# Performance work log

Measured on AMD Instinct MI355X. Metric: run time of the kernel, lower is better.

Reference implementation:

```python
import jax, jax.numpy as jnp
import numpy as np

V, E, HL, HH, T_STEPS, N_STEPS = 32000, 768, 1024, 768, 5, 3
B, S = 8, 256
EPS = 1e-5


def _ln(x, g, b):
    m = jnp.mean(x, axis=-1, keepdims=True)
    v = jnp.var(x, axis=-1, keepdims=True)
    return (x - m) * jax.lax.rsqrt(v + EPS) * g + b


def _gru(x, h, Wi, bi, Wh, bh, lni_g, lni_b, lnh_g, lnh_b):
    # Wi: [3, in_dim, H]; gates stacked in order (r, z, n)
    xi = jnp.einsum('bd,kdh->kbh', x, Wi) + bi[:, None, :]
    hi = jnp.einsum('bh,khg->kbg', h, Wh) + bh[:, None, :]
    xi = _ln(xi, lni_g[:, None, :], lni_b[:, None, :])
    hi = _ln(hi, lnh_g[:, None, :], lnh_b[:, None, :])
    r = jax.nn.sigmoid(xi[0] + hi[0])
    z = jax.nn.sigmoid(xi[1] + hi[1])
    n = jnp.tanh(xi[2] + r * hi[2])
    return (1.0 - z) * n + z * h


def setup_inputs() -> dict:
    key = jax.random.key(0)
    ks = jax.random.split(key, 12)
    lin = E + HH  # low-level cell input dim (x concat h_h)

    def xavier(k, shape, fan_in, fan_out):
        lim = float(np.sqrt(6.0 / (fan_in + fan_out)))
        return jax.random.uniform(k, shape, jnp.float32, -lim, lim)

    inp = {
        'input_ids': jax.random.randint(ks[0], (B, S), 0, V),
        'emb': xavier(ks[1], (V, E), V, E),
        'ln_emb_g': jnp.ones((E,), jnp.float32),
        'ln_emb_b': jnp.zeros((E,), jnp.float32),
        'low_Wi': xavier(ks[2], (3, lin, HL), lin, HL),
        'low_bi': jnp.zeros((3, HL), jnp.float32),
        'low_Wh': xavier(ks[3], (3, HL, HL), HL, HL),
        'low_bh': jnp.zeros((3, HL), jnp.float32),
        'low_lni_g': jnp.ones((3, HL), jnp.float32),
        'low_lni_b': jnp.zeros((3, HL), jnp.float32),
        'low_lnh_g': jnp.ones((3, HL), jnp.float32),
        'low_lnh_b': jnp.zeros((3, HL), jnp.float32),
        'high_Wi': xavier(ks[4], (3, HL, HH), HL, HH),
        'high_bi': jnp.zeros((3, HH), jnp.float32),
        'high_Wh': xavier(ks[5], (3, HH, HH), HH, HH),
        'high_bh': jnp.zeros((3, HH), jnp.float32),
        'high_lni_g': jnp.ones((3, HH), jnp.float32),
        'high_lni_b': jnp.zeros((3, HH), jnp.float32),
        'high_lnh_g': jnp.ones((3, HH), jnp.float32),
        'high_lnh_b': jnp.zeros((3, HH), jnp.float32),
        'Wout': xavier(ks[6], (HH, V), HH, V),
        'bout': jnp.zeros((V,), jnp.float32),
    }
    return inp


def reference(input_ids, emb, ln_emb_g, ln_emb_b,
              low_Wi, low_bi, low_Wh, low_bh,
              low_lni_g, low_lni_b, low_lnh_g, low_lnh_b,
              high_Wi, high_bi, high_Wh, high_bh,
              high_lni_g, high_lni_b, high_lnh_g, high_lnh_b,
              Wout, bout):
    b = input_ids.shape[0]
    h_l0 = jnp.zeros((b, HL), jnp.float32)
    h_h0 = jnp.zeros((b, HH), jnp.float32)

    def step(carry, ids_t):
        h_l, h_h = carry
        x = _ln(emb[ids_t], ln_emb_g, ln_emb_b)  # [B, E]
        for _ in range(N_STEPS):
            for _ in range(T_STEPS):
                h_l = _gru(jnp.concatenate([x, h_h], axis=-1), h_l,
                           low_Wi, low_bi, low_Wh, low_bh,
                           low_lni_g, low_lni_b, low_lnh_g, low_lnh_b)
            h_h = _gru(h_l, h_h,
                       high_Wi, high_bi, high_Wh, high_bh,
                       high_lni_g, high_lni_b, high_lnh_g, high_lnh_b)
        logits_t = h_h @ Wout + bout  # [B, V]
        return (h_l, h_h), logits_t

    _, logits = jax.lax.scan(step, (h_l0, h_h0), input_ids.T)  # [S, B, V]
    return jnp.transpose(logits, (1, 0, 2))  # [B, S, V]
```

## Files before the change

kernel.cpp:

```cpp
#include <hip/hip_runtime.h>
#include <hip/hip_bf16.h>


#define NWG 128
#define NTH 256
#define EPSV 1e-5f

typedef __attribute__((ext_vector_type(4))) float f32x4;
typedef __attribute__((ext_vector_type(8))) short short8;
typedef unsigned long long u64;

struct PArgs {
  const int* ids; const float* emb; const float* lng; const float* lnb;
  const float* lWi; const float* lbi; const float* lWh; const float* lbh;
  const float* llig; const float* llib; const float* llhg; const float* llhb;
  const float* hWi; const float* hbi; const float* hWh; const float* hbh;
  const float* hlig; const float* hlib; const float* hlhg; const float* hlhb;
  int* arr; int* rel; u64* statsG; u64* sredG; float* hlR; float* hhR;
  __hip_bfloat16* hist; float* WiT; float* hWiT; float* hWhT;
};

__device__ __forceinline__ float sigm(float x) { return 1.f / (1.f + __expf(-x)); }
__device__ __forceinline__ float tanh_f(float x) {
  x = fminf(15.f, fmaxf(-15.f, x));
  float e = __expf(2.f * x);
  return (e - 1.f) / (e + 1.f);
}
__device__ __forceinline__ void ast(float* p, float v) {
  __hip_atomic_store(p, v, __ATOMIC_RELAXED, __HIP_MEMORY_SCOPE_AGENT);
}
__device__ __forceinline__ int aldi(const int* p) {
  return __hip_atomic_load(p, __ATOMIC_RELAXED, __HIP_MEMORY_SCOPE_AGENT);
}
__device__ __forceinline__ u64 aldu(const u64* p) {
  return __hip_atomic_load(p, __ATOMIC_RELAXED, __HIP_MEMORY_SCOPE_AGENT);
}
__device__ __forceinline__ void astu(u64* p, u64 v) {
  __hip_atomic_store(p, v, __ATOMIC_RELAXED, __HIP_MEMORY_SCOPE_AGENT);
}
__device__ __forceinline__ void asti(int* p, int v) {
  __hip_atomic_store(p, v, __ATOMIC_RELAXED, __HIP_MEMORY_SCOPE_AGENT);
}
__device__ __forceinline__ void ald4x2(const float* p0, const float* p1,
                                       float4& a, float4& b) {
  asm volatile(
      "global_load_dwordx4 %0, %2, off sc1\n\t"
      "global_load_dwordx4 %1, %3, off sc1\n\t"
      "s_waitcnt vmcnt(0)"
      : "=&v"(a), "=&v"(b)
      : "v"(p0), "v"(p1)
      : "memory");
}
__device__ __forceinline__ void ald4x4(const float* p0, const float* p1,
                                       const float* p2, const float* p3,
                                       float4& a, float4& b, float4& c, float4& d) {
  asm volatile(
      "global_load_dwordx4 %0, %4, off sc1\n\t"
      "global_load_dwordx4 %1, %5, off sc1\n\t"
      "global_load_dwordx4 %2, %6, off sc1\n\t"
      "global_load_dwordx4 %3, %7, off sc1\n\t"
      "s_waitcnt vmcnt(0)"
      : "=&v"(a), "=&v"(b), "=&v"(c), "=&v"(d)
      : "v"(p0), "v"(p1), "v"(p2), "v"(p3)
      : "memory");
}
__device__ __forceinline__ void ald4x8(const float* p0, const float* p1,
                                       const float* p2, const float* p3,
                                       const float* p4, const float* p5,
                                       const float* p6, const float* p7,
                                       float4& a, float4& b, float4& c, float4& d,
                                       float4& e, float4& f, float4& g, float4& h) {
  asm volatile(
      "global_load_dwordx4 %0, %8, off sc1\n\t"
      "global_load_dwordx4 %1, %9, off sc1\n\t"
      "global_load_dwordx4 %2, %10, off sc1\n\t"
      "global_load_dwordx4 %3, %11, off sc1\n\t"
      "global_load_dwordx4 %4, %12, off sc1\n\t"
      "global_load_dwordx4 %5, %13, off sc1\n\t"
      "global_load_dwordx4 %6, %14, off sc1\n\t"
      "global_load_dwordx4 %7, %15, off sc1\n\t"
      "s_waitcnt vmcnt(0)"
      : "=&v"(a), "=&v"(b), "=&v"(c), "=&v"(d),
        "=&v"(e), "=&v"(f), "=&v"(g), "=&v"(h)
      : "v"(p0), "v"(p1), "v"(p2), "v"(p3),
        "v"(p4), "v"(p5), "v"(p6), "v"(p7)
      : "memory");
}

__global__ void __launch_bounds__(NTH) hrm_recur(PArgs P) {
  const int tid = threadIdx.x;

  if (blockIdx.x == NWG) {
    __shared__ float mbuf[192][4];
    __shared__ int mok;
    auto mevent = [&](int e, int lo, int n, float invD, int par) -> bool {
      if (tid < 64) {
        const u64* ap = (const u64*)P.arr + tid;
        int lim = 1 << 22, good = 1;
        for (;;) {
          u64 v = aldu(ap);
          int a0 = (int)(unsigned)(v & 0xffffffffull);
          int a1 = (int)(unsigned)(v >> 32);
          if (__all(a0 >= e && a1 >= e)) break;
          if (--lim == 0) { good = 0; break; }
          __builtin_amdgcn_s_sleep(1);
        }
        if (tid == 0) mok = good;
      }
      __syncthreads();
      bool good = (mok != 0);
      if (good && n > 0) {
        const int rpn = n >> 1;
        const int Q = (n == 48) ? 8 : 16;
        const int wpq = 128 / Q;
        if (tid < rpn * Q) {
          int rp = (lo >> 1) + tid / Q, q = tid % Q;
          const float* b0 = (const float*)(P.statsG + (size_t)par * 128 * 48);
          float4 s; s.x = 0.f; s.y = 0.f; s.z = 0.f; s.w = 0.f;
          #pragma unroll
          for (int blk = 0; blk < 2; ++blk) {
            if (blk == 1 && wpq == 8) break;
            int w0 = q * wpq + blk * 8;
            float4 t0,t1,t2,t3,t4,t5,t6,t7;
            ald4x8(b0 + ((size_t)(w0+0)*48 + rp*2)*2, b0 + ((size_t)(w0+1)*48 + rp*2)*2,
                   b0 + ((size_t)(w0+2)*48 + rp*2)*2, b0 + ((size_t)(w0+3)*48 + rp*2)*2,
                   b0 + ((size_t)(w0+4)*48 + rp*2)*2, b0 + ((size_t)(w0+5)*48 + rp*2)*2,
                   b0 + ((size_t)(w0+6)*48 + rp*2)*2, b0 + ((size_t)(w0+7)*48 + rp*2)*2,
                   t0,t1,t2,t3,t4,t5,t6,t7);
            s.x += t0.x+t1.x+t2.x+t3.x+t4.x+t5.x+t6.x+t7.x;
            s.y += t0.y+t1.y+t2.y+t3.y+t4.y+t5.y+t6.y+t7.y;
            s.z += t0.z+t1.z+t2.z+t3.z+t4.z+t5.z+t6.z+t7.z;
            s.w += t0.w+t1.w+t2.w+t3.w+t4.w+t5.w+t6.w+t7.w;
          }
          mbuf[tid][0] = s.x; mbuf[tid][1] = s.y; mbuf[tid][2] = s.z; mbuf[tid][3] = s.w;
        }
        __syncthreads();
        if (tid < n) {
          int rpl = tid >> 1, comp = tid & 1;
          const int Q2 = (n == 48) ? 8 : 16;
          float s1 = 0.f, s2 = 0.f;
          for (int q = 0; q < Q2; ++q) {
            s1 += mbuf[rpl * Q2 + q][comp * 2 + 0];
            s2 += mbuf[rpl * Q2 + q][comp * 2 + 1];
          }
          float m = s1 * invD;
          float rs = rsqrtf(s2 * invD - m * m + EPSV);
          union { u64 u; float f[2]; } c; c.f[0] = m; c.f[1] = rs;
          astu(P.sredG + (size_t)par * 48 + lo + tid, c.u);
        }
        asm volatile("s_waitcnt vmcnt(0)" ::: "memory");
        __syncthreads();
      }
      int pub = good ? e : (1 << 30);
      if (tid < 8) asti(P.rel + tid * 16, pub);
      return good;
    };

    if (!mevent(1, 0, 0, 0.f, 0)) return;
    int rr = 0;
    #pragma unroll 1
    for (int t = 0; t < 256; ++t) {
      #pragma unroll 1
      for (int nn = 0; nn < 3; ++nn) {
        ++rr;
        if (!mevent(2*rr, 0, 48, 1.f/1024.f, rr & 1)) return;
        if (!mevent(2*rr + 1, 0, 0, 0.f, 0)) return;
        #pragma unroll 1
        for (int it = 1; it < 5; ++it) {
          ++rr;
          if (!mevent(2*rr, 24, 24, 1.f/1024.f, rr & 1)) return;
          if (!mevent(2*rr + 1, 0, 0, 0.f, 0)) return;
        }
        ++rr;
        if (!mevent(2*rr, 0, 48, 1.f/768.f, rr & 1)) return;
        if (!mevent(2*rr + 1, 0, 0, 0.f, 0)) return;
      }
    }
    return;
  }

  __shared__ float WhS[24 * 1024];
  __shared__ float Bb[8 * 1024];
  __shared__ float XW[24 * 8];
  __shared__ float xiNs[24 * 8];
  __shared__ float stg[2][24 * 8];
  __shared__ float sred[96];
  __shared__ float xm[8], xrs[8];
  __shared__ int idsh[8];
  __shared__ int okf;

  const int wg = blockIdx.x;
  const int ks = tid & 31, cg = tid >> 5;
  const int lj8 = wg * 8, lj6 = wg * 6;
  const int rep = wg & 3;

  auto arrive = [&](int e) {
    asm volatile("s_waitcnt vmcnt(0)" ::: "memory");
    __syncthreads();
    if (tid == 0) asti(P.arr + wg, e);
  };
  auto wwait = [&](int e) -> bool {
    if (tid == 0) {
      const int* rp = P.rel + (wg & 7) * 16;
      int lim = 1 << 22, v = 0;
      do {
        v = aldi(rp);
        if (v >= e) break;
        __builtin_amdgcn_s_sleep(1);
      } while (--lim);
      okf = (lim != 0 && v < (1 << 29)) ? 1 : 0;
    }
    __syncthreads();
    return okf != 0;
  };

  auto stage_hl = [&]() {
    const float* base = P.hlR + (size_t)rep * 8192 + tid * 4;
    float4 t0,t1,t2,t3,t4,t5,t6,t7;
    ald4x8(base + 0*1024, base + 1*1024, base + 2*1024, base + 3*1024,
           base + 4*1024, base + 5*1024, base + 6*1024, base + 7*1024,
           t0,t1,t2,t3,t4,t5,t6,t7);
    *(float4*)&Bb[0*1024 + tid*4] = t0; *(float4*)&Bb[1*1024 + tid*4] = t1;
    *(float4*)&Bb[2*1024 + tid*4] = t2; *(float4*)&Bb[3*1024 + tid*4] = t3;
    *(float4*)&Bb[4*1024 + tid*4] = t4; *(float4*)&Bb[5*1024 + tid*4] = t5;
    *(float4*)&Bb[6*1024 + tid*4] = t6; *(float4*)&Bb[7*1024 + tid*4] = t7;
  };
  auto stage_hh = [&]() {
    const float* base = P.hhR + (size_t)rep * 6144;
    int bi[6], ki[6];
    #pragma unroll
    for (int i = 0; i < 6; ++i) {
      int c = i * 256 + tid; int b = c / 192; int k = (c - b * 192) * 4;
      bi[i] = b; ki[i] = k;
    }
    float4 t0,t1,t2,t3,t4,t5;
    ald4x4(base + bi[0]*768 + ki[0], base + bi[1]*768 + ki[1],
           base + bi[2]*768 + ki[2], base + bi[3]*768 + ki[3], t0,t1,t2,t3);
    ald4x2(base + bi[4]*768 + ki[4], base + bi[5]*768 + ki[5], t4,t5);
    *(float4*)&Bb[bi[0]*1024 + ki[0]] = t0; *(float4*)&Bb[bi[1]*1024 + ki[1]] = t1;
    *(float4*)&Bb[bi[2]*1024 + ki[2]] = t2; *(float4*)&Bb[bi[3]*1024 + ki[3]] = t3;
    *(float4*)&Bb[bi[4]*1024 + ki[4]] = t4; *(float4*)&Bb[bi[5]*1024 + ki[5]] = t5;
  };

  auto gemm_lowh = [&](float (&acc)[3][8]) {
    const int c0 = cg * 3;
    const float* w0p = &WhS[(c0 + 0) * 1024];
    const float* w1p = &WhS[(c0 + 1) * 1024];
    const float* w2p = &WhS[(c0 + 2) * 1024];
    #pragma unroll
    for (int i = 0; i < 8; ++i) {
      int k = i * 128 + ks * 4;
      float4 w0 = *(const float4*)&w0p[k];
      float4 w1 = *(const float4*)&w1p[k];
      float4 w2 = *(const float4*)&w2p[k];
      #pragma unroll
      for (int b = 0; b < 8; ++b) {
        float4 h = *(const float4*)&Bb[b * 1024 + k];
        acc[0][b] += w0.x*h.x + w0.y*h.y + w0.z*h.z + w0.w*h.w;
        acc[1][b] += w1.x*h.x + w1.y*h.y + w1.z*h.z + w1.w*h.w;
        acc[2][b] += w2.x*h.x + w2.y*h.y + w2.z*h.z + w2.w*h.w;
      }
    }
  };
  auto gemm_xih = [&](float (&acc)[3][8]) {
    const float* wp[3];
    #pragma unroll
    for (int cc = 0; cc < 3; ++cc) {
      int c = cg * 3 + cc; int g = c >> 3, jj = c & 7;
      wp[cc] = P.WiT + ((size_t)g * 1024 + lj8 + jj) * 1536 + 768;
    }
    #pragma unroll
    for (int i = 0; i < 6; ++i) {
      int k = i * 128 + ks * 4;
      float4 w0 = *(const float4*)&wp[0][k];
      float4 w1 = *(const float4*)&wp[1][k];
      float4 w2 = *(const float4*)&wp[2][k];
      #pragma unroll
      for (int b = 0; b < 8; ++b) {
        float4 h = *(const float4*)&Bb[b * 1024 + k];
        acc[0][b] += w0.x*h.x + w0.y*h.y + w0.z*h.z + w0.w*h.w;
        acc[1][b] += w1.x*h.x + w1.y*h.y + w1.z*h.z + w1.w*h.w;
        acc[2][b] += w2.x*h.x + w2.y*h.y + w2.z*h.z + w2.w*h.w;
      }
    }
  };
  auto gemm_hxi = [&](float (&acc)[3][8]) {
    if (cg >= 6) return;
    const float* wp[3];
    #pragma unroll
    for (int cc = 0; cc < 3; ++cc) {
      int c = cg * 3 + cc; int g = c / 6, jj = c % 6;
      wp[cc] = P.hWiT + ((size_t)g * 768 + lj6 + jj) * 1024;
    }
    #pragma unroll
    for (int i = 0; i < 8; ++i) {
      int k = i * 128 + ks * 4;
      float4 w0 = *(const float4*)&wp[0][k];
      float4 w1 = *(const float4*)&wp[1][k];
      float4 w2 = *(const float4*)&wp[2][k];
      #pragma unroll
      for (int b = 0; b < 8; ++b) {
        float4 h = *(const float4*)&Bb[b * 1024 + k];
        acc[0][b] += w0.x*h.x + w0.y*h.y + w0.z*h.z + w0.w*h.w;
        acc[1][b] += w1.x*h.x + w1.y*h.y + w1.z*h.z + w1.w*h.w;
        acc[2][b] += w2.x*h.x + w2.y*h.y + w2.z*h.z + w2.w*h.w;
      }
    }
  };
  auto gemm_hhh = [&](float (&acc)[3][8]) {
    if (cg >= 6) return;
    const float* wp[3];
    #pragma unroll
    for (int cc = 0; cc < 3; ++cc) {
      int c = cg * 3 + cc; int g = c / 6, jj = c % 6;
      wp[cc] = P.hWhT + ((size_t)g * 768 + lj6 + jj) * 768;
    }
    #pragma unroll
    for (int i = 0; i < 6; ++i) {
      int k = i * 128 + ks * 4;
      float4 w0 = *(const float4*)&wp[0][k];
      float4 w1 = *(const float4*)&wp[1][k];
      float4 w2 = *(const float4*)&wp[2][k];
      #pragma unroll
      for (int b = 0; b < 8; ++b) {
        float4 h = *(const float4*)&Bb[b * 1024 + k];
        acc[0][b] += w0.x*h.x + w0.y*h.y + w0.z*h.z + w0.w*h.w;
        acc[1][b] += w1.x*h.x + w1.y*h.y + w1.z*h.z + w1.w*h.w;
        acc[2][b] += w2.x*h.x + w2.y*h.y + w2.z*h.z + w2.w*h.w;
      }
    }
  };

  auto redstage = [&](float (&acc)[3][8], int set, const float* bias, int dim,
                      int perg, int jb, bool addXW) {
    #pragma unroll
    for (int cc = 0; cc < 3; ++cc)
      #pragma unroll
      for (int b = 0; b < 8; ++b) {
        float v = acc[cc][b];
        #pragma unroll
        for (int m = 1; m < 32; m <<= 1) v += __shfl_xor(v, m, 64);
        acc[cc][b] = v;
      }
    if ((tid & 31) == 0) {
      int cgl = tid >> 5;
      #pragma unroll
      for (int cc = 0; cc < 3; ++cc) {
        int c = cgl * 3 + cc;
        if (c < perg * 3) {
          int g = (perg == 8) ? (c >> 3) : (c / 6);
          int jj = (perg == 8) ? (c & 7) : (c % 6);
          float bs = bias[g * dim + jb + jj];
          #pragma unroll
          for (int b = 0; b < 8; ++b) {
            float v = acc[cc][b] + bs;
            if (addXW) v += XW[c * 8 + b];
            stg[set][c * 8 + b] = v;
          }
        }
      }
    }
  };

  auto stats_put = [&](int par, int set, int perg) {
    if (tid < 24) {
      int g = tid >> 3, b = tid & 7;
      float s1 = 0.f, s2 = 0.f;
      for (int jj = 0; jj < perg; ++jj) {
        float v = stg[set][(g * perg + jj) * 8 + b];
        s1 += v; s2 += v * v;
      }
      union { u64 u; float f[2]; } c; c.f[0] = s1; c.f[1] = s2;
      astu(P.statsG + ((size_t)par * 128 + wg) * 48 + set * 24 + tid, c.u);
    }
  };
  auto sred_read = [&](int par, int lo, int n) {
    if (tid < n) {
      int row = lo + tid;
      union { u64 u; float f[2]; } c;
      c.u = aldu(P.sredG + (size_t)par * 48 + row);
      int set = row / 24, p = row % 24, g = p >> 3, b = p & 7;
      sred[set * 48 + g * 16 + b * 2] = c.f[0];
      sred[set * 48 + g * 16 + b * 2 + 1] = c.f[1];
    }
    __syncthreads();
  };

  auto gate_low = [&](bool isA) {
    if (tid < 64) {
      int jj = tid & 7, b = tid >> 3; int j = lj8 + jj;
      float xin[3], hin[3];
      #pragma unroll
      for (int g = 0; g < 3; ++g) {
        int c = g * 8 + jj;
        if (isA) {
          float m = sred[g * 16 + b * 2], rs = sred[g * 16 + b * 2 + 1];
          float v = (stg[0][c * 8 + b] - m) * rs * P.llig[g * 1024 + j] + P.llib[g * 1024 + j];
          xiNs[c * 8 + b] = v; xin[g] = v;
        } else {
          xin[g] = xiNs[c * 8 + b];
        }
        float m2 = sred[48 + g * 16 + b * 2], rs2 = sred[48 + g * 16 + b * 2 + 1];
        hin[g] = (stg[1][c * 8 + b] - m2) * rs2 * P.llhg[g * 1024 + j] + P.llhb[g * 1024 + j];
      }
      float rg = sigm(xin[0] + hin[0]);
      float zg = sigm(xin[1] + hin[1]);
      float ng = tanh_f(xin[2] + rg * hin[2]);
      float hold = Bb[b * 1024 + j];
      float hv = (1.f - zg) * ng + zg * hold;
      #pragma unroll
      for (int rp = 0; rp < 4; ++rp) ast(&P.hlR[rp * 8192 + b * 1024 + j], hv);
    }
  };

  auto gate_high = [&](int t, int nn) {
    if (tid < 48) {
      int jj = tid % 6, b = tid / 6; int j = lj6 + jj;
      float xin[3], hin[3];
      #pragma unroll
      for (int g = 0; g < 3; ++g) {
        int c = g * 6 + jj;
        float m = sred[g * 16 + b * 2], rs = sred[g * 16 + b * 2 + 1];
        xin[g] = (stg[0][c * 8 + b] - m) * rs * P.hlig[g * 768 + j] + P.hlib[g * 768 + j];
        float m2 = sred[48 + g * 16 + b * 2], rs2 = sred[48 + g * 16 + b * 2 + 1];
        hin[g] = (stg[1][c * 8 + b] - m2) * rs2 * P.hlhg[g * 768 + j] + P.hlhb[g * 768 + j];
      }
      float rg = sigm(xin[0] + hin[0]);
      float zg = sigm(xin[1] + hin[1]);
      float ng = tanh_f(xin[2] + rg * hin[2]);
      float hold = Bb[b * 1024 + j];
      float hv = (1.f - zg) * ng + zg * hold;
      #pragma unroll
      for (int rp = 0; rp < 4; ++rp) ast(&P.hhR[rp * 6144 + b * 768 + j], hv);
      if (nn == 2) P.hist[((size_t)t * 8 + b) * 768 + j] = __float2bfloat16(hv);
    }
  };

  auto xfun = [&](int tt) {
    int b = tid >> 5, u = tid & 31;
    if (tid < 8) idsh[tid] = P.ids[tid * 256 + tt];
    int id = P.ids[b * 256 + tt];
    const float* e = P.emb + (size_t)id * 768;
    float s1 = 0.f, s2 = 0.f;
    #pragma unroll
    for (int q = 0; q < 24; q += 4) {
      float4 v = *(const float4*)&e[u * 24 + q];
      s1 += v.x + v.y + v.z + v.w;
      s2 += v.x*v.x + v.y*v.y + v.z*v.z + v.w*v.w;
    }
    #pragma unroll
    for (int m = 1; m < 32; m <<= 1) { s1 += __shfl_xor(s1, m, 64); s2 += __shfl_xor(s2, m, 64); }
    if (u == 0) { float mm = s1 / 768.f; xm[b] = mm; xrs[b] = rsqrtf(s2 / 768.f - mm * mm + EPSV); }
    __syncthreads();
    float acc[3][8] = {};
    const float* wp[3];
    #pragma unroll
    for (int cc = 0; cc < 3; ++cc) {
      int c = cg * 3 + cc; int g = c >> 3, jj = c & 7;
      wp[cc] = P.WiT + ((size_t)g * 1024 + lj8 + jj) * 1536;
    }
    int idv[8];
    #pragma unroll
    for (int bb = 0; bb < 8; ++bb) idv[bb] = idsh[bb];
    #pragma unroll
    for (int i = 0; i < 6; ++i) {
      int k = i * 128 + ks * 4;
      float4 w0 = *(const float4*)&wp[0][k];
      float4 w1 = *(const float4*)&wp[1][k];
      float4 w2 = *(const float4*)&wp[2][k];
      float4 gam = *(const float4*)&P.lng[k];
      float4 bet = *(const float4*)&P.lnb[k];
      #pragma unroll
      for (int bb = 0; bb < 8; ++bb) {
        float4 xv = *(const float4*)&P.emb[(size_t)idv[bb] * 768 + k];
        float4 xn;
        xn.x = (xv.x - xm[bb]) * xrs[bb] * gam.x + bet.x;
        xn.y = (xv.y - xm[bb]) * xrs[bb] * gam.y + bet.y;
        xn.z = (xv.z - xm[bb]) * xrs[bb] * gam.z + bet.z;
        xn.w = (xv.w - xm[bb]) * xrs[bb] * gam.w + bet.w;
        acc[0][bb] += w0.x*xn.x + w0.y*xn.y + w0.z*xn.z + w0.w*xn.w;
        acc[1][bb] += w1.x*xn.x + w1.y*xn.y + w1.z*xn.z + w1.w*xn.w;
        acc[2][bb] += w2.x*xn.x + w2.y*xn.y + w2.z*xn.z + w2.w*xn.w;
      }
    }
    #pragma unroll
    for (int cc = 0; cc < 3; ++cc)
      #pragma unroll
      for (int bb = 0; bb < 8; ++bb) {
        float v = acc[cc][bb];
        #pragma unroll
        for (int m = 1; m < 32; m <<= 1) v += __shfl_xor(v, m, 64);
        acc[cc][bb] = v;
      }
    if ((tid & 31) == 0) {
      int cgl = tid >> 5;
      #pragma unroll
      for (int cc = 0; cc < 3; ++cc)
        #pragma unroll
        for (int bb = 0; bb < 8; ++bb)
          XW[(cgl * 3 + cc) * 8 + bb] = acc[cc][bb];
    }
    __syncthreads();
  };

  #pragma unroll 1
  for (int g = 0; g < 3; ++g)
    for (int it = 0; it < 6; ++it) {
      int k = it * 256 + tid;
      const float* src = P.lWi + ((size_t)g * 1536 + k) * 1024 + lj8;
      float4 v0 = *(const float4*)src; float4 v1 = *(const float4*)(src + 4);
      float vv[8] = {v0.x, v0.y, v0.z, v0.w, v1.x, v1.y, v1.z, v1.w};
      for (int jj = 0; jj < 8; ++jj)
        P.WiT[((size_t)g * 1024 + lj8 + jj) * 1536 + k] = vv[jj];
    }
  #pragma unroll 1
  for (int g = 0; g < 3; ++g)
    for (int it = 0; it < 4; ++it) {
      int k = it * 256 + tid;
      const float* src = P.hWi + ((size_t)g * 1024 + k) * 768 + lj6;
      float2 a = *(const float2*)src, b2v = *(const float2*)(src + 2), c2v = *(const float2*)(src + 4);
      float vv[6] = {a.x, a.y, b2v.x, b2v.y, c2v.x, c2v.y};
      for (int jj = 0; jj < 6; ++jj)
        P.hWiT[((size_t)g * 768 + lj6 + jj) * 1024 + k] = vv[jj];
    }
  #pragma unroll 1
  for (int g = 0; g < 3; ++g)
    for (int it = 0; it < 3; ++it) {
      int k = it * 256 + tid;
      const float* src = P.hWh + ((size_t)g * 768 + k) * 768 + lj6;
      float2 a = *(const float2*)src, b2v = *(const float2*)(src + 2), c2v = *(const float2*)(src + 4);
      float vv[6] = {a.x, a.y, b2v.x, b2v.y, c2v.x, c2v.y};
      for (int jj = 0; jj < 6; ++jj)
        P.hWhT[((size_t)g * 768 + lj6 + jj) * 768 + k] = vv[jj];
    }
  #pragma unroll 1
  for (int g = 0; g < 3; ++g)
    for (int it = 0; it < 4; ++it) {
      int k = it * 256 + tid;
      const float* src = P.lWh + ((size_t)g * 1024 + k) * 1024 + lj8;
      float4 v0 = *(const float4*)src; float4 v1 = *(const float4*)(src + 4);
      float vv[8] = {v0.x, v0.y, v0.z, v0.w, v1.x, v1.y, v1.z, v1.w};
      for (int jj = 0; jj < 8; ++jj) WhS[(g * 8 + jj) * 1024 + k] = vv[jj];
    }
  __syncthreads();
  xfun(0);
  arrive(1);
  bool alive = wwait(1);

  int rr = 0;
  #pragma unroll 1
  for (int t = 0; alive && t < 256; ++t) {
    #pragma unroll 1
    for (int nn = 0; nn < 3 && alive; ++nn) {
      ++rr; int par = rr & 1;
      {
        stage_hh(); __syncthreads();
        float accX[3][8] = {};
        gemm_xih(accX);
        redstage(accX, 0, P.lbi, 1024, 8, lj8, true);
        __syncthreads();
        stage_hl(); __syncthreads();
        float accH[3][8] = {};
        gemm_lowh(accH);
        redstage(accH, 1, P.lbh, 1024, 8, lj8, false);
        __syncthreads();
        stats_put(par, 0, 8); stats_put(par, 1, 8);
        arrive(2 * rr);
        alive = wwait(2 * rr); if (!alive) break;
        sred_read(par, 0, 48);
        gate_low(true);
        arrive(2 * rr + 1);
        alive = wwait(2 * rr + 1); if (!alive) break;
      }
      #pragma unroll 1
      for (int it = 1; it < 5 && alive; ++it) {
        ++rr; par = rr & 1;
        stage_hl(); __syncthreads();
        float acc2[3][8] = {};
        gemm_lowh(acc2);
        redstage(acc2, 1, P.lbh, 1024, 8, lj8, false);
        __syncthreads();
        stats_put(par, 1, 8);
        arrive(2 * rr);
        alive = wwait(2 * rr); if (!alive) break;
        sred_read(par, 24, 24);
        gate_low(false);
        arrive(2 * rr + 1);
        alive = wwait(2 * rr + 1); if (!alive) break;
      }
      if (!alive) break;
      ++rr; par = rr & 1;
      {
        stage_hl(); __syncthreads();
        float aX[3][8] = {};
        gemm_hxi(aX);
        redstage(aX, 0, P.hbi, 768, 6, lj6, false);
        __syncthreads();
        stage_hh(); __syncthreads();
        float aH[3][8] = {};
        gemm_hhh(aH);
        redstage(aH, 1, P.hbh, 768, 6, lj6, false);
        __syncthreads();
        stats_put(par, 0, 6); stats_put(par, 1, 6);
        arrive(2 * rr);
        alive = wwait(2 * rr); if (!alive) break;
        sred_read(par, 0, 48);
        gate_high(t, nn);
        if (nn == 2 && t < 255) { __syncthreads(); xfun(t + 1); }
        arrive(2 * rr + 1);
        alive = wwait(2 * rr + 1); if (!alive) break;
      }
    }
  }
}

__global__ void __launch_bounds__(256) wout_t(const float* __restrict__ W,
                                              __hip_bfloat16* __restrict__ WT) {
  __shared__ float T[64][65];
  int n0 = blockIdx.x * 64, k0 = blockIdx.y * 64;
  int tid = threadIdx.x;
  int lane16 = tid & 15, grp = tid >> 4;
  #pragma unroll
  for (int i = 0; i < 4; ++i) {
    int kl = i * 16 + grp; int nl = lane16 * 4;
    float4 v = *(const float4*)&W[(size_t)(k0 + kl) * 32000 + n0 + nl];
    T[kl][nl] = v.x; T[kl][nl + 1] = v.y; T[kl][nl + 2] = v.z; T[kl][nl + 3] = v.w;
  }
  __syncthreads();
  #pragma unroll
  for (int i = 0; i < 4; ++i) {
    int nl = i * 16 + grp; int kl = lane16 * 4;
    union { ushort4 v; __hip_bfloat16 h[4]; } u;
    for (int q = 0; q < 4; ++q) u.h[q] = __float2bfloat16(T[kl + q][nl]);
    *(ushort4*)&WT[(size_t)(n0 + nl) * 768 + k0 + kl] = u.v;
  }
}

__global__ void __launch_bounds__(256) logits_gemm(const __hip_bfloat16* __restrict__ Ah,
                                                   const __hip_bfloat16* __restrict__ Bt,
                                                   const float* __restrict__ bias,
                                                   float* __restrict__ out) {
  __shared__ short As[128 * 64];
  __shared__ short Bs[128 * 64];
  int m0 = blockIdx.y * 128, n0 = blockIdx.x * 128;
  int tid = threadIdx.x, lane = tid & 63, w = tid >> 6;
  int wr = w >> 1, wc = w & 1;
  int r16 = lane & 15, khalf = (lane >> 4) * 8;
  f32x4 acc[4][4];
  #pragma unroll
  for (int i = 0; i < 4; ++i)
    #pragma unroll
    for (int j = 0; j < 4; ++j)
      #pragma unroll
      for (int q = 0; q < 4; ++q) acc[i][j][q] = 0.f;

  for (int kt = 0; kt < 12; ++kt) {
    int k0 = kt * 64;
    __syncthreads();
    #pragma unroll
    for (int it = 0; it < 4; ++it) {
      int f = it * 2048 + tid * 8; int row = f >> 6, col = f & 63;
      *(uint4*)&As[f] = *(const uint4*)&Ah[(size_t)(m0 + row) * 768 + k0 + col];
      *(uint4*)&Bs[f] = *(const uint4*)&Bt[(size_t)(n0 + row) * 768 + k0 + col];
    }
    __syncthreads();
    #pragma unroll
    for (int kk = 0; kk < 64; kk += 32) {
      short8 af[4], bfr[4];
      #pragma unroll
      for (int i = 0; i < 4; ++i)
        af[i] = *(short8*)&As[(wr * 64 + i * 16 + r16) * 64 + kk + khalf];
      #pragma unroll
      for (int j = 0; j < 4; ++j)
        bfr[j] = *(short8*)&Bs[(wc * 64 + j * 16 + r16) * 64 + kk + khalf];
      #pragma unroll
      for (int i = 0; i < 4; ++i)
        #pragma unroll
        for (int j = 0; j < 4; ++j)
          acc[i][j] = __builtin_amdgcn_mfma_f32_16x16x32_bf16(af[i], bfr[j], acc[i][j], 0, 0, 0);
    }
  }
  #pragma unroll
  for (int i = 0; i < 4; ++i)
    #pragma unroll
    for (int j = 0; j < 4; ++j)
      #pragma unroll
      for (int q = 0; q < 4; ++q) {
        int m = m0 + wr * 64 + i * 16 + ((lane >> 4) * 4 + q);
        int n = n0 + wc * 64 + j * 16 + (lane & 15);
        out[(size_t)(m & 7) * 8192000 + (size_t)(m >> 3) * 32000 + n] =
            acc[i][j][q] + bias[n];
      }
}

extern "C" void kernel_launch(void* const* d_in, const int* in_sizes, int n_in,
                              void* d_out, int out_size, void* d_ws, size_t ws_size,
                              hipStream_t stream) {
  (void)in_sizes; (void)n_in; (void)out_size; (void)ws_size;
  char* wsb = (char*)d_ws;
  size_t off = 0;
  auto take = [&](size_t bytes) -> void* {
    void* p = wsb + off;
    off += (bytes + 1023) & ~(size_t)1023;
    return p;
  };
  int* arr      = (int*)take((size_t)128 * 4);
  int* rel      = (int*)take((size_t)8 * 16 * 4);
  float* hlR    = (float*)take((size_t)4 * 8 * 1024 * 4);
  float* hhR    = (float*)take((size_t)4 * 8 * 768 * 4);
  size_t state_bytes = off;
  u64* statsG   = (u64*)take((size_t)2 * 128 * 48 * 8);
  u64* sredG    = (u64*)take((size_t)2 * 48 * 8);
  __hip_bfloat16* hist = (__hip_bfloat16*)take((size_t)2048 * 768 * 2);
  float* WiT    = (float*)take((size_t)3 * 1024 * 1536 * 4);
  float* hWiT   = (float*)take((size_t)3 * 768 * 1024 * 4);
  float* hWhT   = (float*)take((size_t)3 * 768 * 768 * 4);
  __hip_bfloat16* WoutT = (__hip_bfloat16*)take((size_t)32000 * 768 * 2);

  hipMemsetAsync(d_ws, 0, state_bytes, stream);

  wout_t<<<dim3(500, 12), 256, 0, stream>>>((const float*)d_in[20], WoutT);

  PArgs A;
  A.ids = (const int*)d_in[0];   A.emb = (const float*)d_in[1];
  A.lng = (const float*)d_in[2]; A.lnb = (const float*)d_in[3];
  A.lWi = (const float*)d_in[4]; A.lbi = (const float*)d_in[5];
  A.lWh = (const float*)d_in[6]; A.lbh = (const float*)d_in[7];
  A.llig = (const float*)d_in[8];  A.llib = (const float*)d_in[9];
  A.llhg = (const float*)d_in[10]; A.llhb = (const float*)d_in[11];
  A.hWi = (const float*)d_in[12];  A.hbi = (const float*)d_in[13];
  A.hWh = (const float*)d_in[14];  A.hbh = (const float*)d_in[15];
  A.hlig = (const float*)d_in[16]; A.hlib = (const float*)d_in[17];
  A.hlhg = (const float*)d_in[18]; A.hlhb = (const float*)d_in[19];
  A.arr = arr; A.rel = rel; A.statsG = statsG; A.sredG = sredG;
  A.hlR = hlR; A.hhR = hhR;
  A.hist = hist; A.WiT = WiT; A.hWiT = hWiT; A.hWhT = hWhT;

  hrm_recur<<<NWG + 1, NTH, 0, stream>>>(A);

  logits_gemm<<<dim3(250, 16), 256, 0, stream>>>(hist, WoutT,
                                                 (const float*)d_in[21],
                                                 (float*)d_out);
}
```

Measured before the change: 70.98 ms.

## Centralize layernorm and gate computation in master block to halve grid barriers

Worker blocks now push raw pre-norm gate outputs to global buffers and arrive once per GRU step. The dedicated master block gathers the full vectors, computes layernorm statistics with wave shuffles, applies the gates, and broadcasts the new hidden state. This removes the second grid-wide barrier per step and the partial-statistics exchange. In exchange, the single master block serializes the elementwise gate work and adds global traffic for the raw vectors.

```diff
diff --git a/kernel.cpp b/kernel.cpp
--- a/kernel.cpp
+++ b/kernel.cpp
@@ -5,6 +5,7 @@
 #define NWG 128
 #define NTH 256
 #define EPSV 1e-5f
+#define NROUND 4608
 
 typedef __attribute__((ext_vector_type(4))) float f32x4;
 typedef __attribute__((ext_vector_type(8))) short short8;
@@ -16,7 +17,7 @@
   const float* llig; const float* llib; const float* llhg; const float* llhb;
   const float* hWi; const float* hbi; const float* hWh; const float* hbh;
   const float* hlig; const float* hlib; const float* hlhg; const float* hlhb;
-  int* arr; int* rel; u64* statsG; u64* sredG; float* hlR; float* hhR;
+  int* arr; int* rel; float* rawL; float* rawH; float* hlR; float* hhR;
   __hip_bfloat16* hist; float* WiT; float* hWiT; float* hWhT;
 };
 
@@ -26,43 +27,23 @@
   float e = __expf(2.f * x);
   return (e - 1.f) / (e + 1.f);
 }
-__device__ __forceinline__ void ast(float* p, float v) {
-  __hip_atomic_store(p, v, __ATOMIC_RELAXED, __HIP_MEMORY_SCOPE_AGENT);
-}
 __device__ __forceinline__ int aldi(const int* p) {
   return __hip_atomic_load(p, __ATOMIC_RELAXED, __HIP_MEMORY_SCOPE_AGENT);
 }
 __device__ __forceinline__ u64 aldu(const u64* p) {
   return __hip_atomic_load(p, __ATOMIC_RELAXED, __HIP_MEMORY_SCOPE_AGENT);
 }
+__device__ __forceinline__ void asti(int* p, int v) {
+  __hip_atomic_store(p, v, __ATOMIC_RELAXED, __HIP_MEMORY_SCOPE_AGENT);
+}
+__device__ __forceinline__ u64 pk2(float a, float b) {
+  union { u64 u; float f[2]; } c; c.f[0] = a; c.f[1] = b; return c.u;
+}
 __device__ __forceinline__ void astu(u64* p, u64 v) {
   __hip_atomic_store(p, v, __ATOMIC_RELAXED, __HIP_MEMORY_SCOPE_AGENT);
 }
-__device__ __forceinline__ void asti(int* p, int v) {
-  __hip_atomic_store(p, v, __ATOMIC_RELAXED, __HIP_MEMORY_SCOPE_AGENT);
-}
-__device__ __forceinline__ void ald4x2(const float* p0, const float* p1,
-                                       float4& a, float4& b) {
-  asm volatile(
-      "global_load_dwordx4 %0, %2, off sc1\n\t"
-      "global_load_dwordx4 %1, %3, off sc1\n\t"
-      "s_waitcnt vmcnt(0)"
-      : "=&v"(a), "=&v"(b)
-      : "v"(p0), "v"(p1)
-      : "memory");
-}
-__device__ __forceinline__ void ald4x4(const float* p0, const float* p1,
-                                       const float* p2, const float* p3,
-                                       float4& a, float4& b, float4& c, float4& d) {
-  asm volatile(
-      "global_load_dwordx4 %0, %4, off sc1\n\t"
-      "global_load_dwordx4 %1, %5, off sc1\n\t"
-      "global_load_dwordx4 %2, %6, off sc1\n\t"
-      "global_load_dwordx4 %3, %7, off sc1\n\t"
-      "s_waitcnt vmcnt(0)"
-      : "=&v"(a), "=&v"(b), "=&v"(c), "=&v"(d)
-      : "v"(p0), "v"(p1), "v"(p2), "v"(p3)
-      : "memory");
+__device__ __forceinline__ void ast2f(float* p, float a, float b) {
+  astu((u64*)p, pk2(a, b));
 }
 __device__ __forceinline__ void ald4x8(const float* p0, const float* p1,
                                        const float* p2, const float* p3,
@@ -86,108 +67,307 @@
         "v"(p4), "v"(p5), "v"(p6), "v"(p7)
       : "memory");
 }
+__device__ __forceinline__ void ald4x6(const float* p0, const float* p1,
+                                       const float* p2, const float* p3,
+                                       const float* p4, const float* p5,
+                                       float4& a, float4& b, float4& c,
+                                       float4& d, float4& e, float4& f) {
+  asm volatile(
+      "global_load_dwordx4 %0, %6, off sc1\n\t"
+      "global_load_dwordx4 %1, %7, off sc1\n\t"
+      "global_load_dwordx4 %2, %8, off sc1\n\t"
+      "global_load_dwordx4 %3, %9, off sc1\n\t"
+      "global_load_dwordx4 %4, %10, off sc1\n\t"
+      "global_load_dwordx4 %5, %11, off sc1\n\t"
+      "s_waitcnt vmcnt(0)"
+      : "=&v"(a), "=&v"(b), "=&v"(c), "=&v"(d), "=&v"(e), "=&v"(f)
+      : "v"(p0), "v"(p1), "v"(p2), "v"(p3), "v"(p4), "v"(p5)
+      : "memory");
+}
+__device__ __forceinline__ void ald4x4(const float* p0, const float* p1,
+                                       const float* p2, const float* p3,
+                                       float4& a, float4& b, float4& c, float4& d) {
+  asm volatile(
+      "global_load_dwordx4 %0, %4, off sc1\n\t"
+      "global_load_dwordx4 %1, %5, off sc1\n\t"
+      "global_load_dwordx4 %2, %6, off sc1\n\t"
+      "global_load_dwordx4 %3, %7, off sc1\n\t"
+      "s_waitcnt vmcnt(0)"
+      : "=&v"(a), "=&v"(b), "=&v"(c), "=&v"(d)
+      : "v"(p0), "v"(p1), "v"(p2), "v"(p3)
+      : "memory");
+}
+__device__ __forceinline__ void ald4x2(const float* p0, const float* p1,
+                                       float4& a, float4& b) {
+  asm volatile(
+      "global_load_dwordx4 %0, %2, off sc1\n\t"
+      "global_load_dwordx4 %1, %3, off sc1\n\t"
+      "s_waitcnt vmcnt(0)"
+      : "=&v"(a), "=&v"(b)
+      : "v"(p0), "v"(p1)
+      : "memory");
+}
 
 __global__ void __launch_bounds__(NTH) hrm_recur(PArgs P) {
+  __shared__ float smem[38920];
   const int tid = threadIdx.x;
 
   if (blockIdx.x == NWG) {
-    __shared__ float mbuf[192][4];
-    __shared__ int mok;
-    auto mevent = [&](int e, int lo, int n, float invD, int par) -> bool {
+    float* xiN = smem;
+    float* hL  = smem + 24576;
+    float* hH  = smem + 32768;
+    int* mokp  = (int*)(smem + 38912);
+    const int b = tid >> 5, l = tid & 31;
+
+    for (int i = tid; i < 8192; i += NTH) hL[i] = 0.f;
+    for (int i = tid; i < 6144; i += NTH) hH[i] = 0.f;
+    __syncthreads();
+    if (tid < 8) asti(P.rel + tid * 16, 1);
+
+    auto load_low_g = [&](int set, int g, float4 (&rv)[4][2]) {
+      const float* base = P.rawL + (((size_t)(set * 3 + g) * 8 + b) * 1024) + l * 8;
+      ald4x8(base, base + 4, base + 256, base + 260,
+             base + 512, base + 516, base + 768, base + 772,
+             rv[0][0], rv[0][1], rv[1][0], rv[1][1],
+             rv[2][0], rv[2][1], rv[3][0], rv[3][1]);
+    };
+    auto load_high_g = [&](int set, int g, float4 (&rv)[3][2]) {
+      const float* base = P.rawH + (((size_t)(set * 3 + g) * 8 + b) * 768) + l * 8;
+      ald4x6(base, base + 4, base + 256, base + 260, base + 512, base + 516,
+             rv[0][0], rv[0][1], rv[1][0], rv[1][1], rv[2][0], rv[2][1]);
+    };
+
+    #pragma unroll 1
+    for (int r = 1; r <= NROUND; ++r) {
       if (tid < 64) {
         const u64* ap = (const u64*)P.arr + tid;
-        int lim = 1 << 22, good = 1;
+        int lim = 1 << 22, g1 = 1;
         for (;;) {
           u64 v = aldu(ap);
           int a0 = (int)(unsigned)(v & 0xffffffffull);
           int a1 = (int)(unsigned)(v >> 32);
-          if (__all(a0 >= e && a1 >= e)) break;
-          if (--lim == 0) { good = 0; break; }
+          if (__all(a0 >= r && a1 >= r)) break;
+          if (--lim == 0) { g1 = 0; break; }
           __builtin_amdgcn_s_sleep(1);
         }
-        if (tid == 0) mok = good;
+        if (tid == 0) *mokp = g1;
       }
       __syncthreads();
-      bool good = (mok != 0);
-      if (good && n > 0) {
-        const int rpn = n >> 1;
-        const int Q = (n == 48) ? 8 : 16;
-        const int wpq = 128 / Q;
-        if (tid < rpn * Q) {
-          int rp = (lo >> 1) + tid / Q, q = tid % Q;
-          const float* b0 = (const float*)(P.statsG + (size_t)par * 128 * 48);
-          float4 s; s.x = 0.f; s.y = 0.f; s.z = 0.f; s.w = 0.f;
-          #pragma unroll
-          for (int blk = 0; blk < 2; ++blk) {
-            if (blk == 1 && wpq == 8) break;
-            int w0 = q * wpq + blk * 8;
-            float4 t0,t1,t2,t3,t4,t5,t6,t7;
-            ald4x8(b0 + ((size_t)(w0+0)*48 + rp*2)*2, b0 + ((size_t)(w0+1)*48 + rp*2)*2,
-                   b0 + ((size_t)(w0+2)*48 + rp*2)*2, b0 + ((size_t)(w0+3)*48 + rp*2)*2,
-                   b0 + ((size_t)(w0+4)*48 + rp*2)*2, b0 + ((size_t)(w0+5)*48 + rp*2)*2,
-                   b0 + ((size_t)(w0+6)*48 + rp*2)*2, b0 + ((size_t)(w0+7)*48 + rp*2)*2,
-                   t0,t1,t2,t3,t4,t5,t6,t7);
-            s.x += t0.x+t1.x+t2.x+t3.x+t4.x+t5.x+t6.x+t7.x;
-            s.y += t0.y+t1.y+t2.y+t3.y+t4.y+t5.y+t6.y+t7.y;
-            s.z += t0.z+t1.z+t2.z+t3.z+t4.z+t5.z+t6.z+t7.z;
-            s.w += t0.w+t1.w+t2.w+t3.w+t4.w+t5.w+t6.w+t7.w;
-          }
-          mbuf[tid][0] = s.x; mbuf[tid][1] = s.y; mbuf[tid][2] = s.z; mbuf[tid][3] = s.w;
+      if (!*mokp) { if (tid < 8) asti(P.rel + tid * 16, 1 << 30); return; }
+
+      const int ph = (r - 1) % 6;
+      const int nn = ((r - 1) / 6) % 3;
+      const int t  = (r - 1) / 18;
+
+      if (ph != 5) {
+        float mm[3], rs[3];
+        if (ph == 0) {
+          float4 rv[3][4][2];
+          #pragma unroll
+          for (int g = 0; g < 3; ++g) load_low_g(0, g, rv[g]);
+          #pragma unroll
+          for (int g = 0; g < 3; ++g) {
+            float s1 = 0.f, s2 = 0.f;
+            #pragma unroll
+            for (int q = 0; q < 4; ++q)
+              #pragma unroll
+              for (int h2 = 0; h2 < 2; ++h2) {
+                float4 v = rv[g][q][h2];
+                s1 += v.x + v.y + v.z + v.w;
+                s2 += v.x*v.x + v.y*v.y + v.z*v.z + v.w*v.w;
+              }
+            #pragma unroll
+            for (int m = 1; m < 32; m <<= 1) { s1 += __shfl_xor(s1, m, 64); s2 += __shfl_xor(s2, m, 64); }
+            float mean = s1 * (1.f / 1024.f);
+            mm[g] = mean; rs[g] = rsqrtf(s2 * (1.f / 1024.f) - mean * mean + EPSV);
+          }
+          #pragma unroll
+          for (int g = 0; g < 3; ++g)
+            #pragma unroll
+            for (int q = 0; q < 4; ++q) {
+              int j0 = q * 256 + l * 8;
+              float4 G0 = *(const float4*)&P.llig[g * 1024 + j0];
+              float4 G1 = *(const float4*)&P.llig[g * 1024 + j0 + 4];
+              float4 B0 = *(const float4*)&P.llib[g * 1024 + j0];
+              float4 B1 = *(const float4*)&P.llib[g * 1024 + j0 + 4];
+              float4 r0 = rv[g][q][0], r1 = rv[g][q][1];
+              float4 x0, x1;
+              x0.x = (r0.x - mm[g]) * rs[g] * G0.x + B0.x;
+              x0.y = (r0.y - mm[g]) * rs[g] * G0.y + B0.y;
+              x0.z = (r0.z - mm[g]) * rs[g] * G0.z + B0.z;
+              x0.w = (r0.w - mm[g]) * rs[g] * G0.w + B0.w;
+              x1.x = (r1.x - mm[g]) * rs[g] * G1.x + B1.x;
+              x1.y = (r1.y - mm[g]) * rs[g] * G1.y + B1.y;
+              x1.z = (r1.z - mm[g]) * rs[g] * G1.z + B1.z;
+              x1.w = (r1.w - mm[g]) * rs[g] * G1.w + B1.w;
+              *(float4*)&xiN[((size_t)g * 8 + b) * 1024 + j0] = x0;
+              *(float4*)&xiN[((size_t)g * 8 + b) * 1024 + j0 + 4] = x1;
+            }
         }
-        __syncthreads();
-        if (tid < n) {
-          int rpl = tid >> 1, comp = tid & 1;
-          const int Q2 = (n == 48) ? 8 : 16;
+        float4 rv[3][4][2];
+        #pragma unroll
+        for (int g = 0; g < 3; ++g) load_low_g(1, g, rv[g]);
+        #pragma unroll
+        for (int g = 0; g < 3; ++g) {
           float s1 = 0.f, s2 = 0.f;
-          for (int q = 0; q < Q2; ++q) {
-            s1 += mbuf[rpl * Q2 + q][comp * 2 + 0];
-            s2 += mbuf[rpl * Q2 + q][comp * 2 + 1];
-          }
-          float m = s1 * invD;
-          float rs = rsqrtf(s2 * invD - m * m + EPSV);
-          union { u64 u; float f[2]; } c; c.f[0] = m; c.f[1] = rs;
-          astu(P.sredG + (size_t)par * 48 + lo + tid, c.u);
+          #pragma unroll
+          for (int q = 0; q < 4; ++q)
+            #pragma unroll
+            for (int h2 = 0; h2 < 2; ++h2) {
+              float4 v = rv[g][q][h2];
+              s1 += v.x + v.y + v.z + v.w;
+              s2 += v.x*v.x + v.y*v.y + v.z*v.z + v.w*v.w;
+            }
+          #pragma unroll
+          for (int m = 1; m < 32; m <<= 1) { s1 += __shfl_xor(s1, m, 64); s2 += __shfl_xor(s2, m, 64); }
+          float mean = s1 * (1.f / 1024.f);
+          mm[g] = mean; rs[g] = rsqrtf(s2 * (1.f / 1024.f) - mean * mean + EPSV);
         }
-        asm volatile("s_waitcnt vmcnt(0)" ::: "memory");
-        __syncthreads();
-      }
-      int pub = good ? e : (1 << 30);
-      if (tid < 8) asti(P.rel + tid * 16, pub);
-      return good;
-    };
-
-    if (!mevent(1, 0, 0, 0.f, 0)) return;
-    int rr = 0;
-    #pragma unroll 1
-    for (int t = 0; t < 256; ++t) {
-      #pragma unroll 1
-      for (int nn = 0; nn < 3; ++nn) {
-        ++rr;
-        if (!mevent(2*rr, 0, 48, 1.f/1024.f, rr & 1)) return;
-        if (!mevent(2*rr + 1, 0, 0, 0.f, 0)) return;
-        #pragma unroll 1
-        for (int it = 1; it < 5; ++it) {
-          ++rr;
-          if (!mevent(2*rr, 24, 24, 1.f/1024.f, rr & 1)) return;
-          if (!mevent(2*rr + 1, 0, 0, 0.f, 0)) return;
+        #pragma unroll
+        for (int q = 0; q < 4; ++q) {
+          int j0 = q * 256 + l * 8;
+          float hin[3][8];
+          #pragma unroll
+          for (int g = 0; g < 3; ++g) {
+            float4 G0 = *(const float4*)&P.llhg[g * 1024 + j0];
+            float4 G1 = *(const float4*)&P.llhg[g * 1024 + j0 + 4];
+            float4 B0 = *(const float4*)&P.llhb[g * 1024 + j0];
+            float4 B1 = *(const float4*)&P.llhb[g * 1024 + j0 + 4];
+            float4 r0 = rv[g][q][0], r1 = rv[g][q][1];
+            hin[g][0] = (r0.x - mm[g]) * rs[g] * G0.x + B0.x;
+            hin[g][1] = (r0.y - mm[g]) * rs[g] * G0.y + B0.y;
+            hin[g][2] = (r0.z - mm[g]) * rs[g] * G0.z + B0.z;
+            hin[g][3] = (r0.w - mm[g]) * rs[g] * G0.w + B0.w;
+            hin[g][4] = (r1.x - mm[g]) * rs[g] * G1.x + B1.x;
+            hin[g][5] = (r1.y - mm[g]) * rs[g] * G1.y + B1.y;
+            hin[g][6] = (r1.z - mm[g]) * rs[g] * G1.z + B1.z;
+            hin[g][7] = (r1.w - mm[g]) * rs[g] * G1.w + B1.w;
+          }
+          float nv[8];
+          #pragma unroll
+          for (int i = 0; i < 8; ++i) {
+            int j = j0 + i;
+            float x0 = xiN[(0 * 8 + b) * 1024 + j];
+            float x1 = xiN[(1 * 8 + b) * 1024 + j];
+            float x2 = xiN[(2 * 8 + b) * 1024 + j];
+            float rg = sigm(x0 + hin[0][i]);
+            float zg = sigm(x1 + hin[1][i]);
+            float ng = tanh_f(x2 + rg * hin[2][i]);
+            float ho = hL[b * 1024 + j];
+            nv[i] = (1.f - zg) * ng + zg * ho;
+            hL[b * 1024 + j] = nv[i];
+          }
+          #pragma unroll
+          for (int rp = 0; rp < 4; ++rp) {
+            float* dp = P.hlR + (size_t)rp * 8192 + b * 1024 + j0;
+            ast2f(dp, nv[0], nv[1]); ast2f(dp + 2, nv[2], nv[3]);
+            ast2f(dp + 4, nv[4], nv[5]); ast2f(dp + 6, nv[6], nv[7]);
+          }
         }
-        ++rr;
-        if (!mevent(2*rr, 0, 48, 1.f/768.f, rr & 1)) return;
-        if (!mevent(2*rr + 1, 0, 0, 0.f, 0)) return;
-      }
+      } else {
+        float4 rv0[3][3][2], rv1[3][3][2];
+        float m0[3], r0s[3], m1[3], r1s[3];
+        #pragma unroll
+        for (int g = 0; g < 3; ++g) load_high_g(0, g, rv0[g]);
+        #pragma unroll
+        for (int g = 0; g < 3; ++g) load_high_g(1, g, rv1[g]);
+        #pragma unroll
+        for (int g = 0; g < 3; ++g) {
+          float s1 = 0.f, s2 = 0.f, u1 = 0.f, u2 = 0.f;
+          #pragma unroll
+          for (int q = 0; q < 3; ++q)
+            #pragma unroll
+            for (int h2 = 0; h2 < 2; ++h2) {
+              float4 v = rv0[g][q][h2];
+              s1 += v.x + v.y + v.z + v.w;
+              s2 += v.x*v.x + v.y*v.y + v.z*v.z + v.w*v.w;
+              float4 w = rv1[g][q][h2];
+              u1 += w.x + w.y + w.z + w.w;
+              u2 += w.x*w.x + w.y*w.y + w.z*w.z + w.w*w.w;
+            }
+          #pragma unroll
+          for (int m = 1; m < 32; m <<= 1) {
+            s1 += __shfl_xor(s1, m, 64); s2 += __shfl_xor(s2, m, 64);
+            u1 += __shfl_xor(u1, m, 64); u2 += __shfl_xor(u2, m, 64);
+          }
+          float a = s1 * (1.f / 768.f);
+          m0[g] = a; r0s[g] = rsqrtf(s2 * (1.f / 768.f) - a * a + EPSV);
+          float c = u1 * (1.f / 768.f);
+          m1[g] = c; r1s[g] = rsqrtf(u2 * (1.f / 768.f) - c * c + EPSV);
+        }
+        #pragma unroll
+        for (int q = 0; q < 3; ++q) {
+          int j0 = q * 256 + l * 8;
+          float xin[3][8], hin[3][8];
+          #pragma unroll
+          for (int g = 0; g < 3; ++g) {
+            float4 GA0 = *(const float4*)&P.hlig[g * 768 + j0];
+            float4 GA1 = *(const float4*)&P.hlig[g * 768 + j0 + 4];
+            float4 BA0 = *(const float4*)&P.hlib[g * 768 + j0];
+            float4 BA1 = *(const float4*)&P.hlib[g * 768 + j0 + 4];
+            float4 GB0 = *(const float4*)&P.hlhg[g * 768 + j0];
+            float4 GB1 = *(const float4*)&P.hlhg[g * 768 + j0 + 4];
+            float4 BB0 = *(const float4*)&P.hlhb[g * 768 + j0];
+            float4 BB1 = *(const float4*)&P.hlhb[g * 768 + j0 + 4];
+            float4 a0 = rv0[g][q][0], a1 = rv0[g][q][1];
+            float4 b0 = rv1[g][q][0], b1 = rv1[g][q][1];
+            xin[g][0] = (a0.x - m0[g]) * r0s[g] * GA0.x + BA0.x;
+            xin[g][1] = (a0.y - m0[g]) * r0s[g] * GA0.y + BA0.y;
+            xin[g][2] = (a0.z - m0[g]) * r0s[g] * GA0.z + BA0.z;
+            xin[g][3] = (a0.w - m0[g]) * r0s[g] * GA0.w + BA0.w;
+            xin[g][4] = (a1.x - m0[g]) * r0s[g] * GA1.x + BA1.x;
+            xin[g][5] = (a1.y - m0[g]) * r0s[g] * GA1.y + BA1.y;
+            xin[g][6] = (a1.z - m0[g]) * r0s[g] * GA1.z + BA1.z;
+            xin[g][7] = (a1.w - m0[g]) * r0s[g] * GA1.w + BA1.w;
+            hin[g][0] = (b0.x - m1[g]) * r1s[g] * GB0.x + BB0.x;
+            hin[g][1] = (b0.y - m1[g]) * r1s[g] * GB0.y + BB0.y;
+            hin[g][2] = (b0.z - m1[g]) * r1s[g] * GB0.z + BB0.z;
+            hin[g][3] = (b0.w - m1[g]) * r1s[g] * GB0.w + BB0.w;
+            hin[g][4] = (b1.x - m1[g]) * r1s[g] * GB1.x + BB1.x;
+            hin[g][5] = (b1.y - m1[g]) * r1s[g] * GB1.y + BB1.y;
+            hin[g][6] = (b1.z - m1[g]) * r1s[g] * GB1.z + BB1.z;
+            hin[g][7] = (b1.w - m1[g]) * r1s[g] * GB1.w + BB1.w;
+          }
+          float nv[8];
+          #pragma unroll
+          for (int i = 0; i < 8; ++i) {
+            int j = j0 + i;
+            float rg = sigm(xin[0][i] + hin[0][i]);
+            float zg = sigm(xin[1][i] + hin[1][i]);
+            float ng = tanh_f(xin[2][i] + rg * hin[2][i]);
+            float ho = hH[b * 768 + j];
+            nv[i] = (1.f - zg) * ng + zg * ho;
+            hH[b * 768 + j] = nv[i];
+          }
+          #pragma unroll
+          for (int rp = 0; rp < 4; ++rp) {
+            float* dp = P.hhR + (size_t)rp * 6144 + b * 768 + j0;
+            ast2f(dp, nv[0], nv[1]); ast2f(dp + 2, nv[2], nv[3]);
+            ast2f(dp + 4, nv[4], nv[5]); ast2f(dp + 6, nv[6], nv[7]);
+          }
+          if (nn == 2) {
+            union { ushort4 v[2]; __hip_bfloat16 h[8]; } u;
+            #pragma unroll
+            for (int i = 0; i < 8; ++i) u.h[i] = __float2bfloat16(nv[i]);
+            *(uint4*)&P.hist[((size_t)t * 8 + b) * 768 + j0] = *(uint4*)&u;
+          }
+        }
+      }
+      asm volatile("s_waitcnt vmcnt(0)" ::: "memory");
+      __syncthreads();
+      if (tid < 8) asti(P.rel + tid * 16, r + 1);
     }
     return;
   }
 
-  __shared__ float WhS[24 * 1024];
-  __shared__ float Bb[8 * 1024];
-  __shared__ float XW[24 * 8];
-  __shared__ float xiNs[24 * 8];
-  __shared__ float stg[2][24 * 8];
-  __shared__ float sred[96];
-  __shared__ float xm[8], xrs[8];
-  __shared__ int idsh[8];
-  __shared__ int okf;
+  float* WhS = smem;
+  float* Bb  = smem + 24576;
+  float* stg = smem + 32768;
+  float* XW  = smem + 33152;
+  float* xm  = smem + 33344;
+  float* xrs = smem + 33352;
+  int* idsh  = (int*)(smem + 33360);
+  int* okfp  = (int*)(smem + 33368);
 
   const int wg = blockIdx.x;
   const int ks = tid & 31, cg = tid >> 5;
@@ -208,10 +388,10 @@
         if (v >= e) break;
         __builtin_amdgcn_s_sleep(1);
       } while (--lim);
-      okf = (lim != 0 && v < (1 << 29)) ? 1 : 0;
+      *okfp = (lim != 0 && v < (1 << 29)) ? 1 : 0;
     }
     __syncthreads();
-    return okf != 0;
+    return *okfp != 0;
   };
 
   auto stage_hl = [&]() {
@@ -230,8 +410,8 @@
     int bi[6], ki[6];
     #pragma unroll
     for (int i = 0; i < 6; ++i) {
-      int c = i * 256 + tid; int b = c / 192; int k = (c - b * 192) * 4;
-      bi[i] = b; ki[i] = k;
+      int c = i * 256 + tid; int bq = c / 192; int k = (c - bq * 192) * 4;
+      bi[i] = bq; ki[i] = k;
     }
     float4 t0,t1,t2,t3,t4,t5;
     ald4x4(base + bi[0]*768 + ki[0], base + bi[1]*768 + ki[1],
@@ -254,11 +434,11 @@
       float4 w1 = *(const float4*)&w1p[k];
       float4 w2 = *(const float4*)&w2p[k];
       #pragma unroll
-      for (int b = 0; b < 8; ++b) {
-        float4 h = *(const float4*)&Bb[b * 1024 + k];
-        acc[0][b] += w0.x*h.x + w0.y*h.y + w0.z*h.z + w0.w*h.w;
-        acc[1][b] += w1.x*h.x + w1.y*h.y + w1.z*h.z + w1.w*h.w;
-        acc[2][b] += w2.x*h.x + w2.y*h.y + w2.z*h.z + w2.w*h.w;
+      for (int bq = 0; bq < 8; ++bq) {
+        float4 h = *(const float4*)&Bb[bq * 1024 + k];
+        acc[0][bq] += w0.x*h.x + w0.y*h.y + w0.z*h.z + w0.w*h.w;
+        acc[1][bq] += w1.x*h.x + w1.y*h.y + w1.z*h.z + w1.w*h.w;
+        acc[2][bq] += w2.x*h.x + w2.y*h.y + w2.z*h.z + w2.w*h.w;
       }
     }
   };
@@ -276,11 +456,11 @@
       float4 w1 = *(const float4*)&wp[1][k];
       float4 w2 = *(const float4*)&wp[2][k];
       #pragma unroll
-      for (int b = 0; b < 8; ++b) {
-        float4 h = *(const float4*)&Bb[b * 1024 + k];
-        acc[0][b] += w0.x*h.x + w0.y*h.y + w0.z*h.z + w0.w*h.w;
-        acc[1][b] += w1.x*h.x + w1.y*h.y + w1.z*h.z + w1.w*h.w;
-        acc[2][b] += w2.x*h.x + w2.y*h.y + w2.z*h.z + w2.w*h.w;
+      for (int bq = 0; bq < 8; ++bq) {
+        float4 h = *(const float4*)&Bb[bq * 1024 + k];
+        acc[0][bq] += w0.x*h.x + w0.y*h.y + w0.z*h.z + w0.w*h.w;
+        acc[1][bq] += w1.x*h.x + w1.y*h.y + w1.z*h.z + w1.w*h.w;
+        acc[2][bq] += w2.x*h.x + w2.y*h.y + w2.z*h.z + w2.w*h.w;
       }
     }
   };
@@ -299,11 +479,11 @@
       float4 w1 = *(const float4*)&wp[1][k];
       float4 w2 = *(const float4*)&wp[2][k];
       #pragma unroll
-      for (int b = 0; b < 8; ++b) {
-        float4 h = *(const float4*)&Bb[b * 1024 + k];
-        acc[0][b] += w0.x*h.x + w0.y*h.y + w0.z*h.z + w0.w*h.w;
-        acc[1][b] += w1.x*h.x + w1.y*h.y + w1.z*h.z + w1.w*h.w;
-        acc[2][b] += w2.x*h.x + w2.y*h.y + w2.z*h.z + w2.w*h.w;
+      for (int bq = 0; bq < 8; ++bq) {
+        float4 h = *(const float4*)&Bb[bq * 1024 + k];
+        acc[0][bq] += w0.x*h.x + w0.y*h.y + w0.z*h.z + w0.w*h.w;
+        acc[1][bq] += w1.x*h.x + w1.y*h.y + w1.z*h.z + w1.w*h.w;
+        acc[2][bq] += w2.x*h.x + w2.y*h.y + w2.z*h.z + w2.w*h.w;
       }
     }
   };
@@ -322,11 +502,11 @@
       float4 w1 = *(const float4*)&wp[1][k];
       float4 w2 = *(const float4*)&wp[2][k];
       #pragma unroll
-      for (int b = 0; b < 8; ++b) {
-        float4 h = *(const float4*)&Bb[b * 1024 + k];
-        acc[0][b] += w0.x*h.x + w0.y*h.y + w0.z*h.z + w0.w*h.w;
-        acc[1][b] += w1.x*h.x + w1.y*h.y + w1.z*h.z + w1.w*h.w;
-        acc[2][b] += w2.x*h.x + w2.y*h.y + w2.z*h.z + w2.w*h.w;
+      for (int bq = 0; bq < 8; ++bq) {
+        float4 h = *(const float4*)&Bb[bq * 1024 + k];
+        acc[0][bq] += w0.x*h.x + w0.y*h.y + w0.z*h.z + w0.w*h.w;
+        acc[1][bq] += w1.x*h.x + w1.y*h.y + w1.z*h.z + w1.w*h.w;
+        acc[2][bq] += w2.x*h.x + w2.y*h.y + w2.z*h.z + w2.w*h.w;
       }
     }
   };
@@ -336,11 +516,11 @@
     #pragma unroll
     for (int cc = 0; cc < 3; ++cc)
       #pragma unroll
-      for (int b = 0; b < 8; ++b) {
-        float v = acc[cc][b];
+      for (int bq = 0; bq < 8; ++bq) {
+        float v = acc[cc][bq];
         #pragma unroll
         for (int m = 1; m < 32; m <<= 1) v += __shfl_xor(v, m, 64);
-        acc[cc][b] = v;
+        acc[cc][bq] = v;
       }
     if ((tid & 31) == 0) {
       int cgl = tid >> 5;
@@ -352,94 +532,42 @@
           int jj = (perg == 8) ? (c & 7) : (c % 6);
           float bs = bias[g * dim + jb + jj];
           #pragma unroll
-          for (int b = 0; b < 8; ++b) {
-            float v = acc[cc][b] + bs;
-            if (addXW) v += XW[c * 8 + b];
-            stg[set][c * 8 + b] = v;
+          for (int bq = 0; bq < 8; ++bq) {
+            float v = acc[cc][bq] + bs;
+            if (addXW) v += XW[c * 8 + bq];
+            stg[set * 192 + c * 8 + bq] = v;
           }
         }
       }
     }
   };
 
-  auto stats_put = [&](int par, int set, int perg) {
+  auto push_rawL = [&](int s) {
     if (tid < 24) {
-      int g = tid >> 3, b = tid & 7;
-      float s1 = 0.f, s2 = 0.f;
-      for (int jj = 0; jj < perg; ++jj) {
-        float v = stg[set][(g * perg + jj) * 8 + b];
-        s1 += v; s2 += v * v;
-      }
-      union { u64 u; float f[2]; } c; c.f[0] = s1; c.f[1] = s2;
-      astu(P.statsG + ((size_t)par * 128 + wg) * 48 + set * 24 + tid, c.u);
-    }
-  };
-  auto sred_read = [&](int par, int lo, int n) {
-    if (tid < n) {
-      int row = lo + tid;
-      union { u64 u; float f[2]; } c;
-      c.u = aldu(P.sredG + (size_t)par * 48 + row);
-      int set = row / 24, p = row % 24, g = p >> 3, b = p & 7;
-      sred[set * 48 + g * 16 + b * 2] = c.f[0];
-      sred[set * 48 + g * 16 + b * 2 + 1] = c.f[1];
-    }
-    __syncthreads();
-  };
-
-  auto gate_low = [&](bool isA) {
-    if (tid < 64) {
-      int jj = tid & 7, b = tid >> 3; int j = lj8 + jj;
-      float xin[3], hin[3];
-      #pragma unroll
-      for (int g = 0; g < 3; ++g) {
-        int c = g * 8 + jj;
-        if (isA) {
-          float m = sred[g * 16 + b * 2], rs = sred[g * 16 + b * 2 + 1];
-          float v = (stg[0][c * 8 + b] - m) * rs * P.llig[g * 1024 + j] + P.llib[g * 1024 + j];
-          xiNs[c * 8 + b] = v; xin[g] = v;
-        } else {
-          xin[g] = xiNs[c * 8 + b];
-        }
-        float m2 = sred[48 + g * 16 + b * 2], rs2 = sred[48 + g * 16 + b * 2 + 1];
-        hin[g] = (stg[1][c * 8 + b] - m2) * rs2 * P.llhg[g * 1024 + j] + P.llhb[g * 1024 + j];
-      }
-      float rg = sigm(xin[0] + hin[0]);
-      float zg = sigm(xin[1] + hin[1]);
-      float ng = tanh_f(xin[2] + rg * hin[2]);
-      float hold = Bb[b * 1024 + j];
-      float hv = (1.f - zg) * ng + zg * hold;
-      #pragma unroll
-      for (int rp = 0; rp < 4; ++rp) ast(&P.hlR[rp * 8192 + b * 1024 + j], hv);
-    }
-  };
-
-  auto gate_high = [&](int t, int nn) {
-    if (tid < 48) {
-      int jj = tid % 6, b = tid / 6; int j = lj6 + jj;
-      float xin[3], hin[3];
-      #pragma unroll
-      for (int g = 0; g < 3; ++g) {
-        int c = g * 6 + jj;
-        float m = sred[g * 16 + b * 2], rs = sred[g * 16 + b * 2 + 1];
-        xin[g] = (stg[0][c * 8 + b] - m) * rs * P.hlig[g * 768 + j] + P.hlib[g * 768 + j];
-        float m2 = sred[48 + g * 16 + b * 2], rs2 = sred[48 + g * 16 + b * 2 + 1];
-        hin[g] = (stg[1][c * 8 + b] - m2) * rs2 * P.hlhg[g * 768 + j] + P.hlhb[g * 768 + j];
-      }
-      float rg = sigm(xin[0] + hin[0]);
-      float zg = sigm(xin[1] + hin[1]);
-      float ng = tanh_f(xin[2] + rg * hin[2]);
-      float hold = Bb[b * 1024 + j];
-      float hv = (1.f - zg) * ng + zg * hold;
-      #pragma unroll
-      for (int rp = 0; rp < 4; ++rp) ast(&P.hhR[rp * 6144 + b * 768 + j], hv);
-      if (nn == 2) P.hist[((size_t)t * 8 + b) * 768 + j] = __float2bfloat16(hv);
+      int g = tid >> 3, bb = tid & 7;
+      const float* sp = stg + s * 192 + g * 64 + bb;
+      float* dp = P.rawL + (((size_t)(s * 3 + g) * 8 + bb) * 1024) + lj8;
+      ast2f(dp,     sp[0],  sp[8]);
+      ast2f(dp + 2, sp[16], sp[24]);
+      ast2f(dp + 4, sp[32], sp[40]);
+      ast2f(dp + 6, sp[48], sp[56]);
+    }
+  };
+  auto push_rawH = [&](int s) {
+    if (tid < 24) {
+      int g = tid >> 3, bb = tid & 7;
+      const float* sp = stg + s * 192 + g * 48 + bb;
+      float* dp = P.rawH + (((size_t)(s * 3 + g) * 8 + bb) * 768) + lj6;
+      ast2f(dp,     sp[0],  sp[8]);
+      ast2f(dp + 2, sp[16], sp[24]);
+      ast2f(dp + 4, sp[32], sp[40]);
     }
   };
 
   auto xfun = [&](int tt) {
-    int b = tid >> 5, u = tid & 31;
+    int bq = tid >> 5, u = tid & 31;
     if (tid < 8) idsh[tid] = P.ids[tid * 256 + tt];
-    int id = P.ids[b * 256 + tt];
+    int id = P.ids[bq * 256 + tt];
     const float* e = P.emb + (size_t)id * 768;
     float s1 = 0.f, s2 = 0.f;
     #pragma unroll
@@ -450,7 +578,7 @@
     }
     #pragma unroll
     for (int m = 1; m < 32; m <<= 1) { s1 += __shfl_xor(s1, m, 64); s2 += __shfl_xor(s2, m, 64); }
-    if (u == 0) { float mm = s1 / 768.f; xm[b] = mm; xrs[b] = rsqrtf(s2 / 768.f - mm * mm + EPSV); }
+    if (u == 0) { float mm = s1 / 768.f; xm[bq] = mm; xrs[bq] = rsqrtf(s2 / 768.f - mm * mm + EPSV); }
     __syncthreads();
     float acc[3][8] = {};
     const float* wp[3];
@@ -544,15 +672,14 @@
     }
   __syncthreads();
   xfun(0);
-  arrive(1);
-  bool alive = wwait(1);
-
-  int rr = 0;
+
+  int r = 1;
+  bool alive = true;
   #pragma unroll 1
-  for (int t = 0; alive && t < 256; ++t) {
+  for (int t = 0; t < 256 && alive; ++t) {
     #pragma unroll 1
     for (int nn = 0; nn < 3 && alive; ++nn) {
-      ++rr; int par = rr & 1;
+      alive = wwait(r); if (!alive) break;
       {
         stage_hh(); __syncthreads();
         float accX[3][8] = {};
@@ -564,32 +691,22 @@
         gemm_lowh(accH);
         redstage(accH, 1, P.lbh, 1024, 8, lj8, false);
         __syncthreads();
-        stats_put(par, 0, 8); stats_put(par, 1, 8);
-        arrive(2 * rr);
-        alive = wwait(2 * rr); if (!alive) break;
-        sred_read(par, 0, 48);
-        gate_low(true);
-        arrive(2 * rr + 1);
-        alive = wwait(2 * rr + 1); if (!alive) break;
+        push_rawL(0); push_rawL(1);
+        arrive(r); ++r;
       }
       #pragma unroll 1
-      for (int it = 1; it < 5 && alive; ++it) {
-        ++rr; par = rr & 1;
+      for (int it = 1; it < 5; ++it) {
+        alive = wwait(r); if (!alive) break;
         stage_hl(); __syncthreads();
         float acc2[3][8] = {};
         gemm_lowh(acc2);
         redstage(acc2, 1, P.lbh, 1024, 8, lj8, false);
         __syncthreads();
-        stats_put(par, 1, 8);
-        arrive(2 * rr);
-        alive = wwait(2 * rr); if (!alive) break;
-        sred_read(par, 24, 24);
-        gate_low(false);
-        arrive(2 * rr + 1);
-        alive = wwait(2 * rr + 1); if (!alive) break;
+        push_rawL(1);
+        arrive(r); ++r;
       }
       if (!alive) break;
-      ++rr; par = rr & 1;
+      alive = wwait(r); if (!alive) break;
       {
         stage_hl(); __syncthreads();
         float aX[3][8] = {};
@@ -601,14 +718,9 @@
         gemm_hhh(aH);
         redstage(aH, 1, P.hbh, 768, 6, lj6, false);
         __syncthreads();
-        stats_put(par, 0, 6); stats_put(par, 1, 6);
-        arrive(2 * rr);
-        alive = wwait(2 * rr); if (!alive) break;
-        sred_read(par, 0, 48);
-        gate_high(t, nn);
-        if (nn == 2 && t < 255) { __syncthreads(); xfun(t + 1); }
-        arrive(2 * rr + 1);
-        alive = wwait(2 * rr + 1); if (!alive) break;
+        push_rawH(0); push_rawH(1);
+        arrive(r); ++r;
+        if (nn == 2 && t < 255) xfun(t + 1);
       }
     }
   }
@@ -704,17 +816,17 @@
     off += (bytes + 1023) & ~(size_t)1023;
     return p;
   };
-  int* arr      = (int*)take((size_t)128 * 4);
-  int* rel      = (int*)take((size_t)8 * 16 * 4);
-  float* hlR    = (float*)take((size_t)4 * 8 * 1024 * 4);
-  float* hhR    = (float*)take((size_t)4 * 8 * 768 * 4);
+  int* arr    = (int*)take((size_t)128 * 4);
+  int* rel    = (int*)take((size_t)8 * 16 * 4);
+  float* hlR  = (float*)take((size_t)4 * 8 * 1024 * 4);
+  float* hhR  = (float*)take((size_t)4 * 8 * 768 * 4);
   size_t state_bytes = off;
-  u64* statsG   = (u64*)take((size_t)2 * 128 * 48 * 8);
-  u64* sredG    = (u64*)take((size_t)2 * 48 * 8);
+  float* rawL = (float*)take((size_t)2 * 3 * 8 * 1024 * 4);
+  float* rawH = (float*)take((size_t)2 * 3 * 8 * 768 * 4);
   __hip_bfloat16* hist = (__hip_bfloat16*)take((size_t)2048 * 768 * 2);
-  float* WiT    = (float*)take((size_t)3 * 1024 * 1536 * 4);
-  float* hWiT   = (float*)take((size_t)3 * 768 * 1024 * 4);
-  float* hWhT   = (float*)take((size_t)3 * 768 * 768 * 4);
+  float* WiT  = (float*)take((size_t)3 * 1024 * 1536 * 4);
+  float* hWiT = (float*)take((size_t)3 * 768 * 1024 * 4);
+  float* hWhT = (float*)take((size_t)3 * 768 * 768 * 4);
   __hip_bfloat16* WoutT = (__hip_bfloat16*)take((size_t)32000 * 768 * 2);
 
   hipMemsetAsync(d_ws, 0, state_bytes, stream);
@@ -732,7 +844,7 @@
   A.hWh = (const float*)d_in[14];  A.hbh = (const float*)d_in[15];
   A.hlig = (const float*)d_in[16]; A.hlib = (const float*)d_in[17];
   A.hlhg = (const float*)d_in[18]; A.hlhb = (const float*)d_in[19];
-  A.arr = arr; A.rel = rel; A.statsG = statsG; A.sredG = sredG;
+  A.arr = arr; A.rel = rel; A.rawL = rawL; A.rawH = rawH;
   A.hlR = hlR; A.hhR = hhR;
   A.hist = hist; A.WiT = WiT; A.hWiT = hWiT; A.hWhT = hWhT;
 
```

New measurement: 156.6 ms. 121% more time.
